# Performance work log

Measured on AMD Instinct MI355X. Metric: run time of the kernel, lower is better.

The kernel has to match this reference:

```python
import jax, jax.numpy as jnp
import numpy as np

B, L, D, Z, V, N, C = 4, 4096, 1024, 128, 1024, 16, 128
STD = 0.02
LN_EPS = 1e-5


def setup_inputs() -> dict:
    ks = jax.random.split(jax.random.key(0), 12)
    f32 = jnp.float32
    return {
        "x": jax.random.normal(ks[0], (B, L, D), dtype=f32),
        "ln1_g": jnp.ones((D,), f32), "ln1_b": jnp.zeros((D,), f32),
        "delta": jax.random.normal(ks[1], (D, N, 1), dtype=f32),
        "alpha": jax.random.normal(ks[2], (D, N, 1), dtype=f32),
        "beta_e": jax.random.normal(ks[3], (D, N, 1), dtype=f32) * STD,
        "gamma_e": jax.random.normal(ks[4], (D, N), dtype=f32),
        "omega": jax.random.normal(ks[5], (D,), dtype=f32) * STD,
        "Wv": jax.random.normal(ks[6], (D, V), dtype=f32) * STD, "bv": jnp.zeros((V,), f32),
        "Wmx": jax.random.normal(ks[7], (D, Z + V + 2 * D), dtype=f32) * STD, "bmx": jnp.zeros((Z + V + 2 * D,), f32),
        "Wh": jax.random.normal(ks[8], (V, D), dtype=f32) * STD, "bh": jnp.zeros((D,), f32),
        "gamma_g": jax.random.normal(ks[9], (2, Z), dtype=f32) * STD, "beta_g": jnp.zeros((2, Z), f32),
        "rpb": jax.random.normal(ks[10], (2 * C - 1,), dtype=f32) * STD,
        "ln2_g": jnp.ones((D,), f32), "ln2_b": jnp.zeros((D,), f32),
        "W1": jax.random.normal(ks[11], (D, 2 * D), dtype=f32) * STD, "b1": jnp.zeros((2 * D,), f32),
        "W2": jax.random.normal(jax.random.fold_in(ks[11], 1), (2 * D, D), dtype=f32) * STD, "b2": jnp.zeros((D,), f32),
    }


def layer_norm(x, g, b):
    m = jnp.mean(x, axis=-1, keepdims=True)
    xc = x - m
    v = jnp.mean(xc * xc, axis=-1, keepdims=True)
    return xc * jax.lax.rsqrt(v + LN_EPS) * g + b


def multi_head_ema(x, delta, alpha, beta_e, gamma_e, omega):
    # x: (B,L,D). Damped EMA SSM (MEGA), unidirectional, via causal FFT conv.
    p = jax.nn.sigmoid(delta)                      # (D,N,1)
    a = jax.nn.sigmoid(alpha)                      # (D,N,1)
    q = 1.0 - p * a                                # decay in (0,1)
    t = jnp.arange(L, dtype=x.dtype)               # (L,)
    vander = t[None, None, :] * jnp.log(q)         # (D,N,L)
    kern = (p * beta_e) * jnp.exp(vander)          # (D,N,L)
    scale = (1.0 / N) ** 0.5
    k = jnp.einsum('dnl,dn->dl', kern, gamma_e * scale)  # (D,L)
    n_fft = 2 * L
    xf = jnp.fft.rfft(x.transpose(0, 2, 1), n=n_fft)     # (B,D,F)
    kf = jnp.fft.rfft(k, n=n_fft)                        # (D,F)
    out = jnp.fft.irfft(xf * kf[None], n=n_fft)[..., :L] # (B,D,L) causal conv
    return out.transpose(0, 2, 1) + x * omega[None, None, :]


def simple_rel_pos_bias(rpb, c):
    # rpb: (2c-1,) -> (c,c) Toeplitz relative-position bias (MEGA 'simple')
    t = jnp.pad(rpb, (0, c))           # (3c-1,)
    t = jnp.tile(t, c)[:-c]            # (c*(3c-2),)
    t = t.reshape(c, 3 * c - 2)
    r = (2 * c - 1) // 2
    return t[:, r: t.shape[1] - r]     # (c,c)


def reference(x, ln1_g, ln1_b, delta, alpha, beta_e, gamma_e, omega, Wv, bv,
              Wmx, bmx, Wh, bh, gamma_g, beta_g, rpb, ln2_g, ln2_b, W1, b1, W2, b2):
    residual = x
    xn = layer_norm(x, ln1_g, ln1_b)                         # prenorm
    v = jax.nn.silu(xn @ Wv + bv)                            # (B,L,V)
    mx = jax.nn.silu(multi_head_ema(xn, delta, alpha, beta_e, gamma_e, omega))
    base = mx @ Wmx + bmx                                    # (B,L,D+Z+V+D)
    u = jax.nn.sigmoid(base[..., :D])                        # gate
    zr = jax.nn.silu(base[..., D:D + Z + V])
    hx = base[..., D + Z + V:]                               # (B,L,D)
    z, r = zr[..., :Z], zr[..., Z:]                          # (B,L,Z),(B,L,V)
    zz = z[..., None, :] * gamma_g + beta_g                  # (B,L,2,Z)
    q, k = zz[..., 0, :], zz[..., 1, :]
    K = L // C
    qc = q.reshape(B, K, C, Z) * (Z ** -0.5)
    kc = k.reshape(B, K, C, Z)
    vc = v.reshape(B, K, C, V)
    bias = simple_rel_pos_bias(rpb, C)                       # (C,C)
    scores = jnp.einsum('bkcz,bkdz->bkcd', qc, kc) + bias    # (B,K,C,C)
    attn = jax.nn.softmax(scores, axis=-1)
    h = jnp.einsum('bkcd,bkdv->bkcv', attn, vc).reshape(B, L, V)
    h = jax.nn.silu(hx + (h * r) @ Wh + bh)                  # (B,L,D)
    out = residual + u * (h - residual)                      # addcmul gate
    # FFN residual block (prenorm, residual 'R')
    y = layer_norm(out, ln2_g, ln2_b)
    y = jax.nn.silu(y @ W1 + b1) @ W2 + b2
    return out + y
```

## Files before the change

kernel.cpp:

```cpp
#include <hip/hip_runtime.h>
#include <hip/hip_bf16.h>

typedef __attribute__((ext_vector_type(8))) short bf16x8;
typedef __attribute__((ext_vector_type(4))) float f32x4;

#define DEV static __device__ __forceinline__

#define VMW(n) asm volatile("s_waitcnt vmcnt(" #n ")" ::: "memory")
#define BARX   asm volatile("s_barrier" ::: "memory")

DEV float bf2f(unsigned short u) {
    unsigned int x = ((unsigned int)u) << 16;
    return __builtin_bit_cast(float, x);
}
DEV unsigned short f2bf(float f) {
    unsigned int x = __builtin_bit_cast(unsigned int, f);
    unsigned int r = x + 0x7fffu + ((x >> 16) & 1u);
    return (unsigned short)(r >> 16);
}
DEV float sigmoidf_(float x) { return 1.f / (1.f + __expf(-x)); }
DEV float siluf_(float x)    { return x / (1.f + __expf(-x)); }

DEV void llds16(const unsigned short* g, unsigned short* l) {
    __builtin_amdgcn_global_load_lds((const __attribute__((address_space(1))) void*)g,
                                     (__attribute__((address_space(3))) void*)l, 16, 0, 0);
}

DEV void swz_xy(int& bx, int& by) {
    int gx = gridDim.x;
    int ychunk = gridDim.y >> 3;
    int n = blockIdx.y * gx + blockIdx.x;
    int idx = n >> 3;
    bx = idx / ychunk;
    by = (n & 7) * ychunk + (idx % ychunk);
}

DEV void mfma256(const unsigned short* __restrict__ A, const unsigned short* __restrict__ Bt,
                 int lda, int ldb, int KT, unsigned short* lds, f32x4 (&acc)[8][4])
{
    const int tid  = threadIdx.x;
    const int lane = tid & 63;
    const int w    = tid >> 6;
    const int wr   = (w >> 2) << 6;
    const int wc   = (w & 3) << 5;
    const int mr   = lane & 15;
    const int kq   = (lane >> 4) << 4;
    const int srow = tid >> 3;
    const int sw   = ((tid & 7) ^ (srow & 7)) << 3;

    auto stA = [&](int b, int kt, int h) {
        const unsigned short* g = A + (size_t)(h * 128 + srow) * lda + kt * 64 + sw;
        unsigned short* d = lds + b * 32768 + h * 8192 + tid * 8;
        llds16(g, d);
        llds16(g + (size_t)64 * lda, d + 4096);
    };
    auto stB = [&](int b, int kt, int h) {
        const unsigned short* g = Bt + (size_t)(h * 128 + srow) * ldb + kt * 64 + sw;
        unsigned short* d = lds + b * 32768 + 16384 + h * 8192 + tid * 8;
        llds16(g, d);
        llds16(g + (size_t)64 * ldb, d + 4096);
    };
    auto ldA = [&](int b, int r, int ks) -> bf16x8 {
        int byte = r * 128 + ((ks * 64 + kq) ^ ((r & 7) << 4));
        return *(const bf16x8*)((const char*)lds + (size_t)b * 65536 + byte);
    };
    auto ldB = [&](int b, int r, int ks) -> bf16x8 {
        int byte = r * 128 + ((ks * 64 + kq) ^ ((r & 7) << 4));
        return *(const bf16x8*)((const char*)lds + (size_t)b * 65536 + 32768 + byte);
    };

    stA(0, 0, 0); stB(0, 0, 0); stB(0, 0, 1); stA(0, 0, 1);

    bf16x8 av[4][2], bA[2][2], bB[2][2];
    for (int kt = 0; kt < KT; ++kt) {
        const int cu = kt & 1, nx = cu ^ 1;
        const bool more = (kt + 1 < KT);
        if (more) { stA(nx, kt + 1, 0); VMW(6); } else VMW(4);
        BARX;
#pragma unroll
        for (int m = 0; m < 4; ++m) { av[m][0] = ldA(cu, wr + m * 16 + mr, 0); av[m][1] = ldA(cu, wr + m * 16 + mr, 1); }
#pragma unroll
        for (int n = 0; n < 2; ++n) { bA[n][0] = ldB(cu, wc + n * 16 + mr, 0); bA[n][1] = ldB(cu, wc + n * 16 + mr, 1); }
        __builtin_amdgcn_s_setprio(1);
#pragma unroll
        for (int m = 0; m < 4; ++m)
#pragma unroll
            for (int n = 0; n < 2; ++n) {
                acc[m][n] = __builtin_amdgcn_mfma_f32_16x16x32_bf16(av[m][0], bA[n][0], acc[m][n], 0, 0, 0);
                acc[m][n] = __builtin_amdgcn_mfma_f32_16x16x32_bf16(av[m][1], bA[n][1], acc[m][n], 0, 0, 0);
            }
        __builtin_amdgcn_s_setprio(0);
        BARX;
        if (more) { stB(nx, kt + 1, 0); VMW(6); } else VMW(2);
        BARX;
#pragma unroll
        for (int n = 0; n < 2; ++n) { bB[n][0] = ldB(cu, 128 + wc + n * 16 + mr, 0); bB[n][1] = ldB(cu, 128 + wc + n * 16 + mr, 1); }
        __builtin_amdgcn_s_setprio(1);
#pragma unroll
        for (int m = 0; m < 4; ++m)
#pragma unroll
            for (int n = 0; n < 2; ++n) {
                acc[m][2 + n] = __builtin_amdgcn_mfma_f32_16x16x32_bf16(av[m][0], bB[n][0], acc[m][2 + n], 0, 0, 0);
                acc[m][2 + n] = __builtin_amdgcn_mfma_f32_16x16x32_bf16(av[m][1], bB[n][1], acc[m][2 + n], 0, 0, 0);
            }
        __builtin_amdgcn_s_setprio(0);
        BARX;
        if (more) { stB(nx, kt + 1, 1); VMW(6); } else VMW(0);
        BARX;
#pragma unroll
        for (int m = 0; m < 4; ++m) { av[m][0] = ldA(cu, 128 + wr + m * 16 + mr, 0); av[m][1] = ldA(cu, 128 + wr + m * 16 + mr, 1); }
        __builtin_amdgcn_s_setprio(1);
#pragma unroll
        for (int m = 0; m < 4; ++m)
#pragma unroll
            for (int n = 0; n < 2; ++n) {
                acc[4 + m][n] = __builtin_amdgcn_mfma_f32_16x16x32_bf16(av[m][0], bA[n][0], acc[4 + m][n], 0, 0, 0);
                acc[4 + m][n] = __builtin_amdgcn_mfma_f32_16x16x32_bf16(av[m][1], bA[n][1], acc[4 + m][n], 0, 0, 0);
            }
        __builtin_amdgcn_s_setprio(0);
        BARX;
        if (more) stA(nx, kt + 1, 1);
        __builtin_amdgcn_s_setprio(1);
#pragma unroll
        for (int m = 0; m < 4; ++m)
#pragma unroll
            for (int n = 0; n < 2; ++n) {
                acc[4 + m][2 + n] = __builtin_amdgcn_mfma_f32_16x16x32_bf16(av[m][0], bB[n][0], acc[4 + m][2 + n], 0, 0, 0);
                acc[4 + m][2 + n] = __builtin_amdgcn_mfma_f32_16x16x32_bf16(av[m][1], bB[n][1], acc[4 + m][2 + n], 0, 0, 0);
            }
        __builtin_amdgcn_s_setprio(0);
        BARX;
    }
}

template <class F>
DEV void stage_rm(unsigned short* lds, const f32x4 (&acc)[8][4], F f)
{
    const int lane = threadIdx.x & 63, w = threadIdx.x >> 6;
    const int wr = (w >> 2) << 6, wc = (w & 3) << 5;
    const int rsub = (lane >> 4) << 2, csub = lane & 15;
#pragma unroll
    for (int i = 0; i < 8; ++i)
#pragma unroll
        for (int j = 0; j < 4; ++j) {
            int rl = ((i >> 2) << 7) + wr + ((i & 3) << 4) + rsub;
            int cl = ((j >> 1) << 7) + wc + ((j & 1) << 4) + csub;
#pragma unroll
            for (int jj = 0; jj < 4; ++jj) {
                int r = rl + jj;
                *(unsigned short*)((char*)lds + r * 512 + ((cl * 2) ^ (((r >> 2) & 3) << 5))) =
                    f(acc[i][j][jj], cl);
            }
        }
}
template <class F>
DEV void stage_cm(unsigned short* lds, const f32x4 (&acc)[8][4], F f)
{
    const int lane = threadIdx.x & 63, w = threadIdx.x >> 6;
    const int wr = (w >> 2) << 6, wc = (w & 3) << 5;
    const int rsub = (lane >> 4) << 2, csub = lane & 15;
#pragma unroll
    for (int i = 0; i < 8; ++i)
#pragma unroll
        for (int j = 0; j < 4; ++j) {
            int rl = ((i >> 2) << 7) + wr + ((i & 3) << 4) + rsub;
            int cl = ((j >> 1) << 7) + wc + ((j & 1) << 4) + csub;
            ushort4 p;
            p.x = f(acc[i][j][0], cl); p.y = f(acc[i][j][1], cl);
            p.z = f(acc[i][j][2], cl); p.w = f(acc[i][j][3], cl);
            *(ushort4*)((char*)lds + cl * 512 + ((rl * 2) ^ ((cl & 3) << 4))) = p;
        }
}
DEV bf16x8 rd_rm(const unsigned short* lds, int row, int cb) {
    return *(const bf16x8*)((const char*)lds + row * 512 + ((cb * 16) ^ (((row >> 2) & 3) << 5)));
}
DEV bf16x8 rd_cm(const unsigned short* lds, int col, int rb) {
    return *(const bf16x8*)((const char*)lds + col * 512 + ((rb * 16) ^ ((col & 3) << 4)));
}

DEV void mfma_loop(const unsigned short* __restrict__ A, const unsigned short* __restrict__ Bt,
                   int lda, int ldb, int K, unsigned short* lds, f32x4 acc[4][4])
{
    const int tid = threadIdx.x;
    const int lane = tid & 63;
    const int wid = tid >> 6;
    const int wm = wid >> 1, wn = wid & 1;
    const int row0 = tid >> 2,         cg0 = (tid & 3) * 8;
    const int row1 = (256 + tid) >> 2, cg1 = (tid & 3) * 8;
    const int dst0 = (tid - lane) * 8;
    const int dst1 = (256 + tid - lane) * 8;

    auto stage = [&](unsigned short* sbuf, int kt) {
        const unsigned short* gA = A + (size_t)kt * 32;
        const unsigned short* gB = Bt + (size_t)kt * 32;
        llds16(gA + (size_t)row0 * lda + cg0, sbuf + dst0);
        llds16(gA + (size_t)row1 * lda + cg1, sbuf + dst1);
        llds16(gB + (size_t)row0 * ldb + cg0, sbuf + 4096 + dst0);
        llds16(gB + (size_t)row1 * ldb + cg1, sbuf + 4096 + dst1);
    };

    const int KT = K >> 5;
    stage(lds, 0);
    __syncthreads();
    const int mr = lane & 15, kr = (lane >> 4) * 8;
    for (int kt = 0; kt < KT; ++kt) {
        unsigned short* sbuf = lds + (kt & 1) * 8192;
        if (kt + 1 < KT) stage(lds + ((kt + 1) & 1) * 8192, kt + 1);
        const unsigned short* sA = sbuf;
        const unsigned short* sB = sbuf + 4096;
        bf16x8 av[4], bv[4];
#pragma unroll
        for (int f = 0; f < 4; ++f) {
            av[f] = *(const bf16x8*)(sA + (wm * 64 + f * 16 + mr) * 32 + kr);
            bv[f] = *(const bf16x8*)(sB + (wn * 64 + f * 16 + mr) * 32 + kr);
        }
#pragma unroll
        for (int fm = 0; fm < 4; ++fm)
#pragma unroll
            for (int fn = 0; fn < 4; ++fn)
                acc[fm][fn] = __builtin_amdgcn_mfma_f32_16x16x32_bf16(av[fm], bv[fn], acc[fm][fn], 0, 0, 0);
        __syncthreads();
    }
}

__global__ void k_transpose(const float* __restrict__ W, unsigned short* __restrict__ Wt, int K, int N)
{
    __shared__ float tile[32][33];
    int n0 = blockIdx.x * 32, k0 = blockIdx.y * 32;
    for (int i = threadIdx.y; i < 32; i += 8)
        tile[i][threadIdx.x] = W[(size_t)(k0 + i) * N + n0 + threadIdx.x];
    __syncthreads();
    for (int i = threadIdx.y; i < 32; i += 8)
        Wt[(size_t)(n0 + i) * K + k0 + threadIdx.x] = f2bf(tile[threadIdx.x][i]);
}

__global__ __launch_bounds__(256) void k_ln(const float* __restrict__ x, const float* __restrict__ g,
                                            const float* __restrict__ b, unsigned short* __restrict__ o)
{
    size_t row = blockIdx.x;
    int tid = threadIdx.x;
    float4 v = ((const float4*)(x + row * 1024))[tid];
    float s = v.x + v.y + v.z + v.w;
    float sq = v.x * v.x + v.y * v.y + v.z * v.z + v.w * v.w;
#pragma unroll
    for (int off = 1; off < 64; off <<= 1) { s += __shfl_xor(s, off); sq += __shfl_xor(sq, off); }
    __shared__ float ls[4], lq[4];
    int wid = tid >> 6;
    if ((tid & 63) == 0) { ls[wid] = s; lq[wid] = sq; }
    __syncthreads();
    s = ls[0] + ls[1] + ls[2] + ls[3];
    sq = lq[0] + lq[1] + lq[2] + lq[3];
    float mean = s * (1.f / 1024.f);
    float var = sq * (1.f / 1024.f) - mean * mean;
    float rstd = rsqrtf(var + 1e-5f);
    float4 gv = ((const float4*)g)[tid];
    float4 bv = ((const float4*)b)[tid];
    ushort4 p;
    p.x = f2bf((v.x - mean) * rstd * gv.x + bv.x);
    p.y = f2bf((v.y - mean) * rstd * gv.y + bv.y);
    p.z = f2bf((v.z - mean) * rstd * gv.z + bv.z);
    p.w = f2bf((v.w - mean) * rstd * gv.w + bv.w);
    ((ushort4*)(o + row * 1024))[tid] = p;
}

#define SEG 128
#define NSEG 32

__global__ __launch_bounds__(64) void k_ema_a(const unsigned short* __restrict__ xn,
                                              const float* __restrict__ delta, const float* __restrict__ alpha,
                                              float* __restrict__ st)
{
    int d = blockIdx.x * 64 + threadIdx.x;
    int s = blockIdx.y, b = blockIdx.z;
    float q[16], h[16];
#pragma unroll
    for (int n = 0; n < 16; ++n) {
        float p = sigmoidf_(delta[d * 16 + n]);
        float a = sigmoidf_(alpha[d * 16 + n]);
        q[n] = 1.f - p * a; h[n] = 0.f;
    }
    const unsigned short* xp = xn + ((size_t)b * 4096 + (size_t)s * SEG) * 1024 + d;
    for (int l = 0; l < SEG; ++l) {
        float xv = bf2f(xp[(size_t)l * 1024]);
#pragma unroll
        for (int n = 0; n < 16; ++n) h[n] = q[n] * h[n] + xv;
    }
    float* sp = st + (size_t)(b * 1024 + d) * 16 * NSEG;
#pragma unroll
    for (int n = 0; n < 16; ++n) sp[n * NSEG + s] = h[n];
}

__global__ void k_ema_b(const float* __restrict__ delta, const float* __restrict__ alpha, float* __restrict__ st)
{
    int gid = blockIdx.x * 256 + threadIdx.x;
    int n = gid & 15, d = (gid >> 4) & 1023;
    float p = sigmoidf_(delta[d * 16 + n]);
    float a = sigmoidf_(alpha[d * 16 + n]);
    float qq = 1.f - p * a;
    float qs = qq;
#pragma unroll
    for (int i = 0; i < 7; ++i) qs *= qs;
    float* sp = st + (size_t)gid * NSEG;
    float A_ = 0.f;
#pragma unroll
    for (int s = 0; s < NSEG; ++s) { float t = sp[s]; sp[s] = A_; A_ = qs * A_ + t; }
}

__global__ __launch_bounds__(64) void k_ema_c(const unsigned short* __restrict__ xn,
                                              const float* __restrict__ delta, const float* __restrict__ alpha,
                                              const float* __restrict__ beta_e, const float* __restrict__ gamma_e,
                                              const float* __restrict__ omega, const float* __restrict__ st,
                                              unsigned short* __restrict__ mxb)
{
    int d = blockIdx.x * 64 + threadIdx.x;
    int s = blockIdx.y, b = blockIdx.z;
    float q[16], c[16], h[16];
    const float* sp = st + (size_t)(b * 1024 + d) * 16 * NSEG;
#pragma unroll
    for (int n = 0; n < 16; ++n) {
        float p = sigmoidf_(delta[d * 16 + n]);
        float a = sigmoidf_(alpha[d * 16 + n]);
        q[n] = 1.f - p * a;
        c[n] = p * beta_e[d * 16 + n] * gamma_e[d * 16 + n] * 0.25f;
        h[n] = sp[n * NSEG + s];
    }
    float om = omega[d];
    const unsigned short* xp = xn + ((size_t)b * 4096 + (size_t)s * SEG) * 1024 + d;
    unsigned short* op = mxb + ((size_t)b * 4096 + (size_t)s * SEG) * 1024 + d;
    for (int l = 0; l < SEG; ++l) {
        float xv = bf2f(xp[(size_t)l * 1024]);
        float o = xv * om;
#pragma unroll
        for (int n = 0; n < 16; ++n) { h[n] = q[n] * h[n] + xv; o += c[n] * h[n]; }
        op[(size_t)l * 1024] = f2bf(siluf_(o));
    }
}

__global__ __launch_bounds__(512, 2) void k_gemm_v2_v(const unsigned short* __restrict__ xn,
                                                      const unsigned short* __restrict__ WvT,
                                                      const float* __restrict__ bv, unsigned short* __restrict__ vt)
{
    __shared__ __align__(16) unsigned short lds[65536];
    int bx, by; swz_xy(bx, by);
    int n0 = bx * 256, m0 = by * 256;
    f32x4 acc[8][4] = {};
    mfma256(xn + (size_t)m0 * 1024, WvT + (size_t)n0 * 1024, 1024, 1024, 16, lds, acc);
    stage_cm(lds, acc, [&](float v, int cl) -> unsigned short {
        return f2bf(siluf_(v + bv[n0 + cl]));
    });
    __syncthreads();
    const int t = threadIdx.x;
#pragma unroll
    for (int it = 0; it < 16; ++it) {
        int col = it * 16 + (t >> 5);
        int rb = t & 31;
        bf16x8 vv = rd_cm(lds, col, rb);
        int grow = m0 + rb * 8;
        size_t off = ((size_t)(grow >> 7) * 1024 + (n0 + col)) * 128 + (grow & 127);
        *(bf16x8*)(vt + off) = vv;
    }
}

__global__ __launch_bounds__(512, 2) void k_gemm_v2_mx(const unsigned short* __restrict__ mx,
                                                       const unsigned short* __restrict__ WmxT,
                                                       const float* __restrict__ bmx,
                                                       const float* __restrict__ gamma_g, const float* __restrict__ beta_g,
                                                       unsigned short* __restrict__ ub, unsigned short* __restrict__ qb,
                                                       unsigned short* __restrict__ kb, unsigned short* __restrict__ rb,
                                                       unsigned short* __restrict__ hxb)
{
    __shared__ __align__(16) unsigned short lds[65536];
    int bx, by; swz_xy(bx, by);
    int n0 = bx * 256, m0 = by * 256;
    f32x4 acc[8][4] = {};
    mfma256(mx + (size_t)m0 * 1024, WmxT + (size_t)n0 * 1024, 1024, 1024, 16, lds, acc);
    stage_rm(lds, acc, [&](float v, int cl) -> unsigned short {
        int gc = n0 + cl;
        if (gc >= 3200) return 0;
        float val = v + bmx[gc];
        if (gc < 1024) return f2bf(sigmoidf_(val));
        if (gc < 2176) return f2bf(siluf_(val));
        return f2bf(val);
    });
    __syncthreads();
    const int t = threadIdx.x;
#pragma unroll
    for (int it = 0; it < 16; ++it) {
        int row = it * 16 + (t >> 5);
        int cb = t & 31;
        int gc = n0 + cb * 8;
        if (gc >= 3200) continue;
        bf16x8 vv = rd_rm(lds, row, cb);
        size_t grow = m0 + row;
        if (gc < 1024) {
            *(bf16x8*)(ub + grow * 1024 + gc) = vv;
        } else if (gc < 1152) {
            int zc = gc - 1024;
            bf16x8 qv, kv;
#pragma unroll
            for (int e = 0; e < 8; ++e) {
                float z = bf2f((unsigned short)vv[e]);
                qv[e] = (short)f2bf((z * gamma_g[zc + e] + beta_g[zc + e]) * 0.088388347648318447f);
                kv[e] = (short)f2bf(z * gamma_g[128 + zc + e] + beta_g[128 + zc + e]);
            }
            *(bf16x8*)(qb + grow * 128 + zc) = qv;
            *(bf16x8*)(kb + grow * 128 + zc) = kv;
        } else if (gc < 2176) {
            *(bf16x8*)(rb + grow * 1024 + (gc - 1152)) = vv;
        } else {
            *(bf16x8*)(hxb + grow * 1024 + (gc - 2176)) = vv;
        }
    }
}

__global__ __launch_bounds__(256) void k_attn(const unsigned short* __restrict__ qb,
                                              const unsigned short* __restrict__ kb,
                                              const float* __restrict__ rpb, unsigned short* __restrict__ attn)
{
    __shared__ __align__(16) union U { unsigned short stage[16384]; unsigned short sc[128 * 132]; } sh;
    int bc = blockIdx.x;
    size_t t0 = (size_t)bc * 128;
    f32x4 acc[4][4] = {};
    mfma_loop(qb + t0 * 128, kb + t0 * 128, 128, 128, 128, sh.stage, acc);
    int tid = threadIdx.x, lane = tid & 63, wid = tid >> 6, wm = wid >> 1, wn = wid & 1;
#pragma unroll
    for (int fm = 0; fm < 4; ++fm)
#pragma unroll
        for (int fn = 0; fn < 4; ++fn) {
            int r = wm * 64 + fm * 16 + ((lane >> 4) << 2);
            int c = wn * 64 + fn * 16 + (lane & 15);
#pragma unroll
            for (int j = 0; j < 4; ++j) sh.sc[(r + j) * 132 + c] = f2bf(acc[fm][fn][j]);
        }
    __syncthreads();
    int row = tid >> 1, half = tid & 1;
    const unsigned short* srow = sh.sc + row * 132 + half * 64;
    const float* bp = rpb + 127 - row + half * 64;
    float v[64];
    float mxv = -1e30f;
#pragma unroll
    for (int i = 0; i < 64; ++i) { float s = bf2f(srow[i]) + bp[i]; v[i] = s; mxv = fmaxf(mxv, s); }
    mxv = fmaxf(mxv, __shfl_xor(mxv, 1));
    float sum = 0.f;
#pragma unroll
    for (int i = 0; i < 64; ++i) { float e = __expf(v[i] - mxv); v[i] = e; sum += e; }
    sum += __shfl_xor(sum, 1);
    float inv = 1.f / sum;
    unsigned short* arow = attn + ((size_t)bc * 128 + row) * 128 + half * 64;
#pragma unroll
    for (int i = 0; i < 64; ++i) arow[i] = f2bf(v[i] * inv);
}

__global__ __launch_bounds__(256) void k_gemm_pv(const unsigned short* __restrict__ attn,
                                                 const unsigned short* __restrict__ vt,
                                                 unsigned short* __restrict__ rhr)
{
    __shared__ __align__(16) unsigned short lds[16384];
    int bc = blockIdx.z;
    int n0 = blockIdx.x * 128;
    f32x4 acc[4][4] = {};
    mfma_loop(attn + (size_t)bc * 16384, vt + (size_t)bc * 131072 + (size_t)n0 * 128, 128, 128, 128, lds, acc);
    int lane = threadIdx.x & 63, wid = threadIdx.x >> 6, wm = wid >> 1, wn = wid & 1;
#pragma unroll
    for (int fm = 0; fm < 4; ++fm)
#pragma unroll
        for (int fn = 0; fn < 4; ++fn) {
            int rowb = wm * 64 + fm * 16 + ((lane >> 4) << 2);
            int col = n0 + wn * 64 + fn * 16 + (lane & 15);
#pragma unroll
            for (int j = 0; j < 4; ++j) {
                size_t m = (size_t)bc * 128 + rowb + j;
                size_t off = m * 1024 + col;
                rhr[off] = f2bf(acc[fm][fn][j] * bf2f(rhr[off]));
            }
        }
}

__global__ __launch_bounds__(512, 2) void k_gemm_v2_out(const unsigned short* __restrict__ hr,
                                                        const unsigned short* __restrict__ WhT,
                                                        const float* __restrict__ bh,
                                                        const unsigned short* __restrict__ hxb,
                                                        const unsigned short* __restrict__ ub,
                                                        const float* __restrict__ x, float* __restrict__ outp)
{
    __shared__ __align__(16) unsigned short lds[65536];
    int bx, by; swz_xy(bx, by);
    int n0 = bx * 256, m0 = by * 256;
    f32x4 acc[8][4] = {};
    mfma256(hr + (size_t)m0 * 1024, WhT + (size_t)n0 * 1024, 1024, 1024, 16, lds, acc);
    const int lane = threadIdx.x & 63, w = threadIdx.x >> 6;
    const int wr = (w >> 2) << 6, wc = (w & 3) << 5;
    const int rsub = (lane >> 4) << 2, csub = lane & 15;
#pragma unroll
    for (int i = 0; i < 8; ++i)
#pragma unroll
        for (int j = 0; j < 4; ++j) {
            int rowb = m0 + ((i >> 2) << 7) + wr + ((i & 3) << 4) + rsub;
            int col = n0 + ((j >> 1) << 7) + wc + ((j & 1) << 4) + csub;
            float bias = bh[col];
#pragma unroll
            for (int jj = 0; jj < 4; ++jj) {
                size_t off = (size_t)(rowb + jj) * 1024 + col;
                float g = acc[i][j][jj] + bias + bf2f(hxb[off]);
                float h2 = siluf_(g);
                float xv = x[off];
                outp[off] = xv + bf2f(ub[off]) * (h2 - xv);
            }
        }
}

__global__ __launch_bounds__(512, 2) void k_ffn1_v2(const unsigned short* __restrict__ yn,
                                                    const unsigned short* __restrict__ W1T,
                                                    const float* __restrict__ b1, unsigned short* __restrict__ t1)
{
    __shared__ __align__(16) unsigned short lds[65536];
    int bx, by; swz_xy(bx, by);
    int n0 = bx * 256, m0 = by * 256;
    f32x4 acc[8][4] = {};
    mfma256(yn + (size_t)m0 * 1024, W1T + (size_t)n0 * 1024, 1024, 1024, 16, lds, acc);
    stage_rm(lds, acc, [&](float v, int cl) -> unsigned short {
        return f2bf(siluf_(v + b1[n0 + cl]));
    });
    __syncthreads();
    const int t = threadIdx.x;
#pragma unroll
    for (int it = 0; it < 16; ++it) {
        int row = it * 16 + (t >> 5);
        int cb = t & 31;
        bf16x8 vv = rd_rm(lds, row, cb);
        *(bf16x8*)(t1 + (size_t)(m0 + row) * 2048 + n0 + cb * 8) = vv;
    }
}

__global__ __launch_bounds__(512, 2) void k_ffn2_v2(const unsigned short* __restrict__ t1,
                                                    const unsigned short* __restrict__ W2T,
                                                    const float* __restrict__ b2, float* __restrict__ outp)
{
    __shared__ __align__(16) unsigned short lds[65536];
    int bx, by; swz_xy(bx, by);
    int n0 = bx * 256, m0 = by * 256;
    f32x4 acc[8][4] = {};
    mfma256(t1 + (size_t)m0 * 2048, W2T + (size_t)n0 * 2048, 2048, 2048, 32, lds, acc);
    const int lane = threadIdx.x & 63, w = threadIdx.x >> 6;
    const int wr = (w >> 2) << 6, wc = (w & 3) << 5;
    const int rsub = (lane >> 4) << 2, csub = lane & 15;
#pragma unroll
    for (int i = 0; i < 8; ++i)
#pragma unroll
        for (int j = 0; j < 4; ++j) {
            int rowb = m0 + ((i >> 2) << 7) + wr + ((i & 3) << 4) + rsub;
            int col = n0 + ((j >> 1) << 7) + wc + ((j & 1) << 4) + csub;
            float bias = b2[col];
#pragma unroll
            for (int jj = 0; jj < 4; ++jj) {
                size_t off = (size_t)(rowb + jj) * 1024 + col;
                outp[off] = outp[off] + acc[i][j][jj] + bias;
            }
        }
}

extern "C" void kernel_launch(void* const* d_in, const int* in_sizes, int n_in,
                              void* d_out, int out_size, void* d_ws, size_t ws_size,
                              hipStream_t stream)
{
    (void)in_sizes; (void)n_in; (void)out_size; (void)ws_size;
    const float* x      = (const float*)d_in[0];
    const float* ln1_g  = (const float*)d_in[1];
    const float* ln1_b  = (const float*)d_in[2];
    const float* delta  = (const float*)d_in[3];
    const float* alpha  = (const float*)d_in[4];
    const float* beta_e = (const float*)d_in[5];
    const float* gamma_e= (const float*)d_in[6];
    const float* omega  = (const float*)d_in[7];
    const float* Wv     = (const float*)d_in[8];
    const float* bv     = (const float*)d_in[9];
    const float* Wmx    = (const float*)d_in[10];
    const float* bmx    = (const float*)d_in[11];
    const float* Wh     = (const float*)d_in[12];
    const float* bh     = (const float*)d_in[13];
    const float* gamma_g= (const float*)d_in[14];
    const float* beta_g = (const float*)d_in[15];
    const float* rpb    = (const float*)d_in[16];
    const float* ln2_g  = (const float*)d_in[17];
    const float* ln2_b  = (const float*)d_in[18];
    const float* W1     = (const float*)d_in[19];
    const float* b1     = (const float*)d_in[20];
    const float* W2     = (const float*)d_in[21];
    const float* b2     = (const float*)d_in[22];
    float* outp = (float*)d_out;

    char* w = (char*)d_ws;
    unsigned short* xn   = (unsigned short*)(w + 0);
    unsigned short* at   = (unsigned short*)(w + 0);
    unsigned short* mxb  = (unsigned short*)(w + 33554432);
    unsigned short* t1   = (unsigned short*)(w + 0);
    unsigned short* vt   = (unsigned short*)(w + 67108864);
    unsigned short* ub   = (unsigned short*)(w + 100663296);
    unsigned short* hxb  = (unsigned short*)(w + 134217728);
    unsigned short* rb   = (unsigned short*)(w + 167772160);
    unsigned short* yn   = (unsigned short*)(w + 167772160);
    unsigned short* qb   = (unsigned short*)(w + 201326592);
    unsigned short* kb   = (unsigned short*)(w + 205520896);
    float*          st   = (float*)(w + 201326592);
    unsigned short* WvT  = (unsigned short*)(w + 209715200);
    unsigned short* WmxT = (unsigned short*)(w + 211812352);
    unsigned short* WhT  = (unsigned short*)(w + 218628096);
    unsigned short* W1T  = (unsigned short*)(w + 220725248);
    unsigned short* W2T  = (unsigned short*)(w + 224919552);

    dim3 tb(32, 8);
    k_transpose<<<dim3(32, 32), tb, 0, stream>>>(Wv, WvT, 1024, 1024);
    k_transpose<<<dim3(100, 32), tb, 0, stream>>>(Wmx, WmxT, 1024, 3200);
    k_transpose<<<dim3(32, 32), tb, 0, stream>>>(Wh, WhT, 1024, 1024);
    k_transpose<<<dim3(64, 32), tb, 0, stream>>>(W1, W1T, 1024, 2048);
    k_transpose<<<dim3(32, 64), tb, 0, stream>>>(W2, W2T, 2048, 1024);

    k_ln<<<16384, 256, 0, stream>>>(x, ln1_g, ln1_b, xn);

    k_ema_a<<<dim3(16, NSEG, 4), 64, 0, stream>>>(xn, delta, alpha, st);
    k_ema_b<<<256, 256, 0, stream>>>(delta, alpha, st);
    k_ema_c<<<dim3(16, NSEG, 4), 64, 0, stream>>>(xn, delta, alpha, beta_e, gamma_e, omega, st, mxb);

    k_gemm_v2_v<<<dim3(4, 64), 512, 0, stream>>>(xn, WvT, bv, vt);
    k_gemm_v2_mx<<<dim3(13, 64), 512, 0, stream>>>(mxb, WmxT, bmx, gamma_g, beta_g, ub, qb, kb, rb, hxb);
    k_attn<<<128, 256, 0, stream>>>(qb, kb, rpb, at);
    k_gemm_pv<<<dim3(8, 1, 128), 256, 0, stream>>>(at, vt, rb);
    k_gemm_v2_out<<<dim3(4, 64), 512, 0, stream>>>(rb, WhT, bh, hxb, ub, x, outp);
    k_ln<<<16384, 256, 0, stream>>>(outp, ln2_g, ln2_b, yn);
    k_ffn1_v2<<<dim3(8, 64), 512, 0, stream>>>(yn, W1T, b1, t1);
    k_ffn2_v2<<<dim3(4, 64), 512, 0, stream>>>(t1, W2T, b2, outp);
}
```

Baseline: 644.1 us.

## Prefetch whole next K-tile at loop top with one barrier per iteration

The bf16 MFMA GEMM main loop used to interleave four partial-tile global-to-LDS loads with about seven s_barriers per K step. It now waits for all outstanding loads, takes a single barrier, and issues all eight loads for the next K tile into the other double buffer at once. The loads then overlap with the MFMAs of the whole current tile. LDS read addresses and global pointers are precomputed and advanced incrementally instead of being rebuilt in lambdas. This cuts barrier stalls and address arithmetic, but the vmcnt(0) wait at the top gives up the finer-grained staged overlap the old schedule had.

```diff
diff --git a/kernel.cpp b/kernel.cpp
--- a/kernel.cpp
+++ b/kernel.cpp
@@ -48,39 +48,42 @@
     const int srow = tid >> 3;
     const int sw   = ((tid & 7) ^ (srow & 7)) << 3;
 
-    auto stA = [&](int b, int kt, int h) {
-        const unsigned short* g = A + (size_t)(h * 128 + srow) * lda + kt * 64 + sw;
-        unsigned short* d = lds + b * 32768 + h * 8192 + tid * 8;
-        llds16(g, d);
-        llds16(g + (size_t)64 * lda, d + 4096);
-    };
-    auto stB = [&](int b, int kt, int h) {
-        const unsigned short* g = Bt + (size_t)(h * 128 + srow) * ldb + kt * 64 + sw;
-        unsigned short* d = lds + b * 32768 + 16384 + h * 8192 + tid * 8;
-        llds16(g, d);
-        llds16(g + (size_t)64 * ldb, d + 4096);
-    };
-    auto ldA = [&](int b, int r, int ks) -> bf16x8 {
-        int byte = r * 128 + ((ks * 64 + kq) ^ ((r & 7) << 4));
-        return *(const bf16x8*)((const char*)lds + (size_t)b * 65536 + byte);
-    };
-    auto ldB = [&](int b, int r, int ks) -> bf16x8 {
-        int byte = r * 128 + ((ks * 64 + kq) ^ ((r & 7) << 4));
-        return *(const bf16x8*)((const char*)lds + (size_t)b * 65536 + 32768 + byte);
-    };
-
-    stA(0, 0, 0); stB(0, 0, 0); stB(0, 0, 1); stA(0, 0, 1);
+    const unsigned short* gA0 = A + (size_t)srow * lda + sw;
+    const unsigned short* gA1 = gA0 + (size_t)128 * lda;
+    const unsigned short* gB0 = Bt + (size_t)srow * ldb + sw;
+    const unsigned short* gB1 = gB0 + (size_t)128 * ldb;
+    const size_t a64 = (size_t)64 * lda, b64 = (size_t)64 * ldb;
+    unsigned short* dst = lds + tid * 8;
+
+    const int swz = (mr & 7) << 4;
+    const int offK0 = kq ^ swz;
+    const int offK1 = (64 + kq) ^ swz;
+    const char* pAb = (const char*)lds + (wr + mr) * 128;
+    const char* pBb = (const char*)lds + 32768 + (wc + mr) * 128;
+
+#define STAGE8(NX) do { \
+    unsigned short* d0 = dst + (NX) * 32768; \
+    llds16(gA0, d0);          llds16(gA0 + a64, d0 + 4096);  gA0 += 64; \
+    llds16(gB0, d0 + 16384);  llds16(gB0 + b64, d0 + 20480); gB0 += 64; \
+    llds16(gB1, d0 + 24576);  llds16(gB1 + b64, d0 + 28672); gB1 += 64; \
+    llds16(gA1, d0 + 8192);   llds16(gA1 + a64, d0 + 12288); gA1 += 64; \
+} while (0)
+
+    STAGE8(0);
 
     bf16x8 av[4][2], bA[2][2], bB[2][2];
     for (int kt = 0; kt < KT; ++kt) {
-        const int cu = kt & 1, nx = cu ^ 1;
-        const bool more = (kt + 1 < KT);
-        if (more) { stA(nx, kt + 1, 0); VMW(6); } else VMW(4);
+        VMW(0);
         BARX;
-#pragma unroll
-        for (int m = 0; m < 4; ++m) { av[m][0] = ldA(cu, wr + m * 16 + mr, 0); av[m][1] = ldA(cu, wr + m * 16 + mr, 1); }
-#pragma unroll
-        for (int n = 0; n < 2; ++n) { bA[n][0] = ldB(cu, wc + n * 16 + mr, 0); bA[n][1] = ldB(cu, wc + n * 16 + mr, 1); }
+        if (kt + 1 < KT) STAGE8((kt & 1) ^ 1);
+        const char* pA_ = pAb + (kt & 1) * 65536;
+        const char* pB_ = pBb + (kt & 1) * 65536;
+#pragma unroll
+        for (int m = 0; m < 4; ++m) { av[m][0] = *(const bf16x8*)(pA_ + m * 2048 + offK0);
+                                      av[m][1] = *(const bf16x8*)(pA_ + m * 2048 + offK1); }
+#pragma unroll
+        for (int n = 0; n < 2; ++n) { bA[n][0] = *(const bf16x8*)(pB_ + n * 2048 + offK0);
+                                      bA[n][1] = *(const bf16x8*)(pB_ + n * 2048 + offK1); }
         __builtin_amdgcn_s_setprio(1);
 #pragma unroll
         for (int m = 0; m < 4; ++m)
@@ -90,11 +93,9 @@
                 acc[m][n] = __builtin_amdgcn_mfma_f32_16x16x32_bf16(av[m][1], bA[n][1], acc[m][n], 0, 0, 0);
             }
         __builtin_amdgcn_s_setprio(0);
-        BARX;
-        if (more) { stB(nx, kt + 1, 0); VMW(6); } else VMW(2);
-        BARX;
-#pragma unroll
-        for (int n = 0; n < 2; ++n) { bB[n][0] = ldB(cu, 128 + wc + n * 16 + mr, 0); bB[n][1] = ldB(cu, 128 + wc + n * 16 + mr, 1); }
+#pragma unroll
+        for (int n = 0; n < 2; ++n) { bB[n][0] = *(const bf16x8*)(pB_ + 16384 + n * 2048 + offK0);
+                                      bB[n][1] = *(const bf16x8*)(pB_ + 16384 + n * 2048 + offK1); }
         __builtin_amdgcn_s_setprio(1);
 #pragma unroll
         for (int m = 0; m < 4; ++m)
@@ -104,11 +105,9 @@
                 acc[m][2 + n] = __builtin_amdgcn_mfma_f32_16x16x32_bf16(av[m][1], bB[n][1], acc[m][2 + n], 0, 0, 0);
             }
         __builtin_amdgcn_s_setprio(0);
-        BARX;
-        if (more) { stB(nx, kt + 1, 1); VMW(6); } else VMW(0);
-        BARX;
-#pragma unroll
-        for (int m = 0; m < 4; ++m) { av[m][0] = ldA(cu, 128 + wr + m * 16 + mr, 0); av[m][1] = ldA(cu, 128 + wr + m * 16 + mr, 1); }
+#pragma unroll
+        for (int m = 0; m < 4; ++m) { av[m][0] = *(const bf16x8*)(pA_ + 16384 + m * 2048 + offK0);
+                                      av[m][1] = *(const bf16x8*)(pA_ + 16384 + m * 2048 + offK1); }
         __builtin_amdgcn_s_setprio(1);
 #pragma unroll
         for (int m = 0; m < 4; ++m)
@@ -118,8 +117,6 @@
                 acc[4 + m][n] = __builtin_amdgcn_mfma_f32_16x16x32_bf16(av[m][1], bA[n][1], acc[4 + m][n], 0, 0, 0);
             }
         __builtin_amdgcn_s_setprio(0);
-        BARX;
-        if (more) stA(nx, kt + 1, 1);
         __builtin_amdgcn_s_setprio(1);
 #pragma unroll
         for (int m = 0; m < 4; ++m)
@@ -129,8 +126,9 @@
                 acc[4 + m][2 + n] = __builtin_amdgcn_mfma_f32_16x16x32_bf16(av[m][1], bB[n][1], acc[4 + m][2 + n], 0, 0, 0);
             }
         __builtin_amdgcn_s_setprio(0);
-        BARX;
-    }
+    }
+#undef STAGE8
+    BARX;
 }
 
 template <class F>
```

After: 646.7 us. Within noise of the previous version (+0.4%).
